# Performance work log

Measured on AMD Instinct MI355X. Metric: run time of the kernel, lower is better.

Reference implementation:

```python
import jax, jax.numpy as jnp
import numpy as np

B, P, N = 64, 100, 1000
D, H, QD = 128, 8, 16
NUM_PATCHES = 196
NTOT = N + NUM_PATCHES
SQRT_D = float(np.sqrt(D))   # sqrt_embedding_dim
CLIP = 10.0                  # logit_clipping


def setup_inputs() -> dict:
    key = jax.random.key(0)
    ks = jax.random.split(key, 10)
    return {
        "encoded_last_node": jax.random.normal(ks[0], (B, P, D), jnp.float32),
        "ninf_mask": jnp.zeros((B, P, N), jnp.float32),
        "q_first": jax.random.normal(ks[1], (B, H, P, QD), jnp.float32),
        "k": jax.random.normal(ks[2], (B, H, NTOT, QD), jnp.float32),
        "v": jax.random.normal(ks[3], (B, H, NTOT, QD), jnp.float32),
        "single_head_key": jax.random.normal(ks[4], (B, D, N), jnp.float32),
        "Wq_last": jax.random.normal(ks[5], (D, H * QD), jnp.float32) * 0.05,
        "mh_combine": jax.random.normal(ks[6], (H * QD, D), jnp.float32) * 0.05,
        "edge_bias": jax.random.normal(ks[7], (B, N, N), jnp.float32) * 0.1,
        "current_node": jax.random.randint(ks[8], (B, P), 0, N, jnp.int64),
        "num_patches": NUM_PATCHES,
    }


def reference(encoded_last_node, ninf_mask, q_first, k, v, single_head_key,
              Wq_last, mh_combine, edge_bias, current_node, num_patches):
    b, p, _ = encoded_last_node.shape
    h, qd = q_first.shape[1], q_first.shape[3]

    # q_last = reshape_by_heads(F.linear(x, Wq_last_para))  -> [B,H,P,qd]
    q_last = (encoded_last_node @ Wq_last.T).reshape(b, p, h, qd).transpose(0, 2, 1, 3)
    q = q_first + q_last

    # multi-head attention with mask extended by zero columns for patch tokens
    mask_full = jnp.pad(ninf_mask, ((0, 0), (0, 0), (0, num_patches)))  # [B,P,Ntot]
    score = jnp.einsum('bhpd,bhnd->bhpn', q, k) / jnp.sqrt(jnp.float32(qd))
    weights = jax.nn.softmax(score + mask_full[:, None, :, :], axis=-1)
    out = jnp.einsum('bhpn,bhnd->bhpd', weights, v)
    out_concat = out.transpose(0, 2, 1, 3).reshape(b, p, h * qd)  # [B,P,D]

    mh_atten_out = out_concat @ mh_combine.T                       # [B,P,D]

    # pointer-style single-head score with tanh clipping
    score2 = jnp.einsum('bpd,bdn->bpn', mh_atten_out, single_head_key)
    score_clipped = CLIP * jnp.tanh(score2 / SQRT_D)

    # gather edge bias row for current node: bias[b,p,n] = edge_bias[b, current_node[b,p], n]
    bias_row = jnp.take_along_axis(edge_bias, current_node[:, :, None], axis=1)
    probs = jax.nn.softmax(score_clipped + bias_row + ninf_mask, axis=-1)
    return probs
```

## Files before the change

### kernel.cpp

```cpp
#include <hip/hip_runtime.h>
#include <math.h>

#define BB 64
#define PP 100
#define NN 1000
#define DD 128
#define HH 8
#define QDQ 16
#define NTOT 1196
#define QROWS 16
#define LOG2E 1.44269504088896f
#define EXP2(x) __builtin_amdgcn_exp2f(x)

typedef float f2 __attribute__((ext_vector_type(2)));
typedef short s8v __attribute__((ext_vector_type(8)));
typedef float f16v __attribute__((ext_vector_type(16)));

static __device__ __forceinline__ f2 splat2(float v) { f2 r; r.x = v; r.y = v; return r; }
#define PKFMA(a, b, c) __builtin_elementwise_fma((a), (b), (c))

static __device__ __forceinline__ unsigned pkhi(float a, float b) {
  return (__float_as_uint(a) >> 16) | (__float_as_uint(b) & 0xffff0000u);
}
static __device__ __forceinline__ float truncbf(float a) {
  return __uint_as_float(__float_as_uint(a) & 0xffff0000u);
}
#define MFMA32(a, b, c) __builtin_amdgcn_mfma_f32_32x32x16_bf16((a), (b), (c), 0, 0, 0)

__global__ __launch_bounds__(256) void k_prep(const float* __restrict__ x,
                                              const float* __restrict__ Wq,
                                              const float* __restrict__ qf,
                                              float* __restrict__ qout,
                                              const float* __restrict__ mask,
                                              unsigned short* __restrict__ m2) {
  __shared__ float sw[128 * 65];
  __shared__ float xs[QROWS * DD];
  int tid = threadIdx.x;

  if (blockIdx.x < 400) {
    int row0 = blockIdx.x * QROWS;
    for (int i = tid; i < QROWS * DD / 4; i += 256)
      ((float4*)xs)[i] = ((const float4*)(x + (size_t)row0 * DD))[i];

    int j = tid & 127, rr = tid >> 7;
    float acc[8];
#pragma unroll
    for (int i = 0; i < 8; ++i) acc[i] = 0.f;

    for (int half = 0; half < 2; ++half) {
      __syncthreads();
      for (int idx = tid; idx < 128 * 64; idx += 256) {
        int jj = idx >> 6, dl = idx & 63;
        sw[jj * 65 + dl] = Wq[jj * DD + half * 64 + dl];
      }
      __syncthreads();
#pragma unroll
      for (int ri = 0; ri < 8; ++ri) {
        int r = 2 * ri + rr;
        float a = acc[ri];
#pragma unroll 16
        for (int dl = 0; dl < 64; ++dl)
          a += xs[r * DD + half * 64 + dl] * sw[j * 65 + dl];
        acc[ri] = a;
      }
    }
#pragma unroll
    for (int ri = 0; ri < 8; ++ri) {
      int bp = row0 + 2 * ri + rr;
      int b = bp / PP, p = bp % PP;
      int h = j >> 4, qd = j & 15;
      size_t qi = ((size_t)(b * HH + h) * PP + p) * QDQ + qd;
      qout[qi] = acc[ri] + qf[qi];
    }
  } else {
    int t2 = blockIdx.x - 400;
    int b = t2 >> 7, q = t2 & 127;
    unsigned short* dst = m2 + (size_t)(b * 128 + q) * 1280;
    const float* srow = mask + ((size_t)b * PP + (q < PP ? q : PP - 1)) * NN;
    for (int j = tid; j < 1280; j += 256) {
      int h = j >= 640 ? 1 : 0;
      int jj = j - h * 640;
      float val;
      if (q >= PP || jj >= 598) {
        val = -1e4f;
      } else {
        int n = h * 598 + jj;
        val = (n < NN) ? srow[n] * LOG2E - 20.f : -20.f;
      }
      dst[j] = (unsigned short)(__float_as_uint(val) >> 16);
    }
  }
}

__global__ __launch_bounds__(256) void k_mha(const float* __restrict__ kk,
                                             const float* __restrict__ vv,
                                             const float* __restrict__ qws,
                                             const unsigned short* __restrict__ m2,
                                             float* __restrict__ part) {
  int bid = blockIdx.x;
  int swz = (bid & 7) * 128 + (bid >> 3);
  int bh = swz >> 1, half = swz & 1;
  int b = bh >> 3;
  int tid = threadIdx.x;
  int w = tid >> 6, lane = tid & 63;
  int L = lane >> 5, ln = lane & 31;
  bool lo = (L == 0);

  __shared__ __align__(16) char pool[27264];
  char* KspB = pool;
  char* VThB = pool + 8192;
  char* VTlB = pool + 12288;
  char* QhB  = pool + 16384;
  char* QlB  = pool + 20480;

  {
    const float* qrow = qws + (size_t)bh * (PP * QDQ);
    for (int i = tid; i < 128 * 16; i += 256) {
      int p = i >> 4, qd = i & 15;
      float v = (p < PP) ? qrow[p * QDQ + qd] * (0.25f * LOG2E) : 0.f;
      ((unsigned short*)QhB)[i] = (unsigned short)(__float_as_uint(v) >> 16);
      float rl = v - truncbf(v);
      ((unsigned short*)QlB)[i] = (unsigned short)(__float_as_uint(rl) >> 16);
    }
  }

  const float4* kf4 = (const float4*)kk + (size_t)bh * NTOT * 4;
  const float4* vf4 = (const float4*)vv + (size_t)bh * NTOT * 4;

  f16v Oacc[4];
  float lacc[4];
#pragma unroll
  for (int qt = 0; qt < 4; ++qt) {
    lacc[qt] = 0.f;
#pragma unroll
    for (int r = 0; r < 16; ++r) Oacc[qt][r] = 0.f;
  }
  s8v QhF[4], QlF[4];

  for (int c = 0; c < 5; ++c) {
    __syncthreads();
#pragma unroll
    for (int rep = 0; rep < 2; ++rep) {
      int f = tid + rep * 256;
      int key_l = f >> 2, qd0 = (f & 3) << 2;
      int j = c * 128 + key_l;
      int jc = j < 598 ? j : 597;
      size_t gidx = (size_t)(half * 598 + jc) * 4 + (qd0 >> 2);
      float4 k4 = kf4[gidx];
      unsigned kh01 = pkhi(k4.x, k4.y), kh23 = pkhi(k4.z, k4.w);
      float r0 = k4.x - truncbf(k4.x), r1 = k4.y - truncbf(k4.y);
      float r2 = k4.z - truncbf(k4.z), r3 = k4.w - truncbf(k4.w);
      unsigned kl01 = pkhi(r0, r1), kl23 = pkhi(r2, r3);
      *(uint2*)(KspB + key_l * 64 + qd0 * 2) = make_uint2(kh01, kh23);
      *(uint2*)(KspB + key_l * 64 + 32 + qd0 * 2) = make_uint2(kl01, kl23);
      float4 v4 = vf4[gidx];
      float ve0 = v4.x, ve1 = v4.y, ve2 = v4.z, ve3 = v4.w;
      ((unsigned short*)VThB)[(qd0 + 0) * 128 + key_l] = (unsigned short)(__float_as_uint(ve0) >> 16);
      ((unsigned short*)VThB)[(qd0 + 1) * 128 + key_l] = (unsigned short)(__float_as_uint(ve1) >> 16);
      ((unsigned short*)VThB)[(qd0 + 2) * 128 + key_l] = (unsigned short)(__float_as_uint(ve2) >> 16);
      ((unsigned short*)VThB)[(qd0 + 3) * 128 + key_l] = (unsigned short)(__float_as_uint(ve3) >> 16);
      float w0 = ve0 - truncbf(ve0), w1 = ve1 - truncbf(ve1);
      float w2 = ve2 - truncbf(ve2), w3 = ve3 - truncbf(ve3);
      ((unsigned short*)VTlB)[(qd0 + 0) * 128 + key_l] = (unsigned short)(__float_as_uint(w0) >> 16);
      ((unsigned short*)VTlB)[(qd0 + 1) * 128 + key_l] = (unsigned short)(__float_as_uint(w1) >> 16);
      ((unsigned short*)VTlB)[(qd0 + 2) * 128 + key_l] = (unsigned short)(__float_as_uint(w2) >> 16);
      ((unsigned short*)VTlB)[(qd0 + 3) * 128 + key_l] = (unsigned short)(__float_as_uint(w3) >> 16);
    }
    __syncthreads();
    if (c == 0) {
#pragma unroll
      for (int qt = 0; qt < 4; ++qt) {
        int qr = qt * 32 + ln;
        QhF[qt] = *(const s8v*)(QhB + qr * 32 + L * 16);
        QlF[qt] = *(const s8v*)(QlB + qr * 32 + L * 16);
      }
    }
    int ktb = w * 32;
    s8v KhF = *(const s8v*)(KspB + (ktb + ln) * 64 + L * 16);
    s8v KlF = *(const s8v*)(KspB + (ktb + ln) * 64 + 32 + L * 16);
    int vr = ln & 15;
    s8v VhS0 = *(const s8v*)(VThB + vr * 256 + (ktb + L * 8) * 2);
    s8v VhS1 = *(const s8v*)(VThB + vr * 256 + (ktb + 16 + L * 8) * 2);
    s8v VlS0 = *(const s8v*)(VTlB + vr * 256 + (ktb + L * 8) * 2);
    s8v VlS1 = *(const s8v*)(VTlB + vr * 256 + (ktb + 16 + L * 8) * 2);
    size_t mkey = (size_t)half * 640 + c * 128 + ktb + 4 * L;
#pragma unroll
    for (int qt = 0; qt < 4; ++qt) {
      const unsigned short* mrow = m2 + (size_t)(b * 128 + qt * 32 + ln) * 1280 + mkey;
      f16v acc;
#pragma unroll
      for (int g = 0; g < 4; ++g) {
        uint2 md = *(const uint2*)(mrow + g * 8);
        acc[g * 4 + 0] = __uint_as_float(md.x << 16);
        acc[g * 4 + 1] = __uint_as_float(md.x & 0xffff0000u);
        acc[g * 4 + 2] = __uint_as_float(md.y << 16);
        acc[g * 4 + 3] = __uint_as_float(md.y & 0xffff0000u);
      }
      acc = MFMA32(KhF, QhF[qt], acc);
      acc = MFMA32(KhF, QlF[qt], acc);
      acc = MFMA32(KlF, QhF[qt], acc);
      float p[16];
      float ls = 0.f;
#pragma unroll
      for (int r = 0; r < 16; ++r) { p[r] = EXP2(acc[r]); ls += p[r]; }
      lacc[qt] += ls;
#pragma unroll
      for (int s = 0; s < 2; ++s) {
        unsigned a0 = pkhi(p[8 * s + 0], p[8 * s + 1]), a1 = pkhi(p[8 * s + 2], p[8 * s + 3]);
        unsigned b0 = pkhi(p[8 * s + 4], p[8 * s + 5]), b1 = pkhi(p[8 * s + 6], p[8 * s + 7]);
        unsigned sa0 = __shfl_xor(a0, 32), sa1 = __shfl_xor(a1, 32);
        unsigned sb0 = __shfl_xor(b0, 32), sb1 = __shfl_xor(b1, 32);
        uint4 phu = make_uint4(lo ? a0 : sb0, lo ? a1 : sb1, lo ? sa0 : b0, lo ? sa1 : b1);
        float t0 = p[8 * s + 0] - truncbf(p[8 * s + 0]), t1 = p[8 * s + 1] - truncbf(p[8 * s + 1]);
        float t2 = p[8 * s + 2] - truncbf(p[8 * s + 2]), t3 = p[8 * s + 3] - truncbf(p[8 * s + 3]);
        float t4 = p[8 * s + 4] - truncbf(p[8 * s + 4]), t5 = p[8 * s + 5] - truncbf(p[8 * s + 5]);
        float t6 = p[8 * s + 6] - truncbf(p[8 * s + 6]), t7 = p[8 * s + 7] - truncbf(p[8 * s + 7]);
        unsigned c0 = pkhi(t0, t1), c1 = pkhi(t2, t3);
        unsigned e0 = pkhi(t4, t5), e1 = pkhi(t6, t7);
        unsigned sc0 = __shfl_xor(c0, 32), sc1 = __shfl_xor(c1, 32);
        unsigned se0 = __shfl_xor(e0, 32), se1 = __shfl_xor(e1, 32);
        uint4 plu = make_uint4(lo ? c0 : se0, lo ? c1 : se1, lo ? sc0 : e0, lo ? sc1 : e1);
        s8v APh = *(s8v*)&phu;
        s8v APl = *(s8v*)&plu;
        s8v Vh = s ? VhS1 : VhS0;
        s8v Vl = s ? VlS1 : VlS0;
        Oacc[qt] = MFMA32(APh, Vh, Oacc[qt]);
        Oacc[qt] = MFMA32(APh, Vl, Oacc[qt]);
        Oacc[qt] = MFMA32(APl, Vh, Oacc[qt]);
      }
    }
  }

  float lf[4];
#pragma unroll
  for (int qt = 0; qt < 4; ++qt) lf[qt] = lacc[qt] + __shfl_xor(lacc[qt], 32);

  __syncthreads();
  float* marea = (float*)pool;
  float* larea = (float*)(pool + 25600);
  if (ln < 16) {
#pragma unroll
    for (int qt = 0; qt < 4; ++qt) {
#pragma unroll
      for (int r = 0; r < 16; ++r) {
        int q = qt * 32 + (r & 3) + 8 * (r >> 2) + 4 * L;
        if (q < PP) marea[(w * PP + q) * 16 + ln] = Oacc[qt][r];
      }
    }
  }
  if (lane < 32) {
#pragma unroll
    for (int qt = 0; qt < 4; ++qt) {
      int q = qt * 32 + ln;
      if (q < PP) larea[w * PP + q] = lf[qt];
    }
  }
  __syncthreads();
  for (int idx = tid; idx < PP * 17; idx += 256) {
    int q = idx / 17, e = idx % 17;
    float sv;
    if (e < 16)
      sv = marea[(0 * PP + q) * 16 + e] + marea[(1 * PP + q) * 16 + e]
         + marea[(2 * PP + q) * 16 + e] + marea[(3 * PP + q) * 16 + e];
    else
      sv = larea[0 * PP + q] + larea[1 * PP + q] + larea[2 * PP + q] + larea[3 * PP + q];
    part[((size_t)swz * PP + q) * 17 + e] = sv;
  }
}

__global__ __launch_bounds__(256) void k_combine(const float* __restrict__ part,
                                                 const float* __restrict__ MC,
                                                 float* __restrict__ mh) {
  __shared__ float sw[128 * 65];
  __shared__ float oc[QROWS * DD];
  int tid = threadIdx.x;
  int row0 = blockIdx.x * QROWS;

  for (int i = tid; i < QROWS * DD; i += 256) {
    int r = i >> 7, t = i & 127;
    int bp = row0 + r, b = bp / PP, p = bp % PP;
    int qd = t & 15, h = t >> 4;
    int bh = b * HH + h;
    const float* r0 = part + (((size_t)(bh * 2 + 0)) * PP + p) * 17;
    const float* r1 = part + (((size_t)(bh * 2 + 1)) * PP + p) * 17;
    float A = r0[qd] + r1[qd];
    float L = r0[16] + r1[16];
    oc[i] = A / L;
  }

  int j = tid & 127, rr = tid >> 7;
  float acc[8];
#pragma unroll
  for (int i = 0; i < 8; ++i) acc[i] = 0.f;

  for (int half = 0; half < 2; ++half) {
    __syncthreads();
    for (int idx = tid; idx < 128 * 64; idx += 256) {
      int jj = idx >> 6, dl = idx & 63;
      sw[jj * 65 + dl] = MC[jj * DD + half * 64 + dl];
    }
    __syncthreads();
#pragma unroll
    for (int ri = 0; ri < 8; ++ri) {
      int r = 2 * ri + rr;
      float a = acc[ri];
#pragma unroll 16
      for (int dl = 0; dl < 64; ++dl)
        a += oc[r * DD + half * 64 + dl] * sw[j * 65 + dl];
      acc[ri] = a;
    }
  }
#pragma unroll
  for (int ri = 0; ri < 8; ++ri) {
    int bp = row0 + 2 * ri + rr;
    mh[(size_t)bp * DD + j] = acc[ri];
  }
}

__global__ __launch_bounds__(256) void k_score2(const float* __restrict__ mh,
                                                const float* __restrict__ shk,
                                                float* __restrict__ sc) {
  int bid = blockIdx.x;
  int swz = (bid & 7) * 128 + (bid >> 3);
  int b = swz >> 4, nt = swz & 15;
  int tid = threadIdx.x; int nl = tid & 31, pg = tid >> 5;
  __shared__ float A[PP * 132];
  for (int idx = tid; idx < PP * DD; idx += 256)
    A[(idx >> 7) * 132 + (idx & 127)] = mh[(size_t)b * PP * DD + idx];
  __syncthreads();

  int na = nt * 64 + nl, nb2 = na + 32;
  int nca = na < NN ? na : NN - 1, ncb = nb2 < NN ? nb2 : NN - 1;
  const float* S = shk + (size_t)b * DD * NN;
  f2 accv[13];
#pragma unroll
  for (int i = 0; i < 13; ++i) accv[i] = splat2(0.f);

  for (int d = 0; d < DD; d += 4) {
    f2 s0, s1, s2, s3;
    s0.x = S[(size_t)(d + 0) * NN + nca]; s0.y = S[(size_t)(d + 0) * NN + ncb];
    s1.x = S[(size_t)(d + 1) * NN + nca]; s1.y = S[(size_t)(d + 1) * NN + ncb];
    s2.x = S[(size_t)(d + 2) * NN + nca]; s2.y = S[(size_t)(d + 2) * NN + ncb];
    s3.x = S[(size_t)(d + 3) * NN + nca]; s3.y = S[(size_t)(d + 3) * NN + ncb];
#pragma unroll
    for (int i = 0; i < 13; ++i) {
      int p = pg + (i << 3);
      if (p < PP) {
        const float4 a4 = *(const float4*)&A[p * 132 + d];
        accv[i] = PKFMA(splat2(a4.x), s0, accv[i]);
        accv[i] = PKFMA(splat2(a4.y), s1, accv[i]);
        accv[i] = PKFMA(splat2(a4.z), s2, accv[i]);
        accv[i] = PKFMA(splat2(a4.w), s3, accv[i]);
      }
    }
  }
#pragma unroll
  for (int i = 0; i < 13; ++i) {
    int p = pg + (i << 3);
    if (p < PP) {
      size_t base = ((size_t)b * PP + p) * NN;
      if (na < NN) sc[base + na] = accv[i].x;
      if (nb2 < NN) sc[base + nb2] = accv[i].y;
    }
  }
}

__global__ __launch_bounds__(256) void k_finsm(const float* __restrict__ sc,
                                               const float* __restrict__ eb,
                                               const int* __restrict__ cn,
                                               const float* __restrict__ mask,
                                               float* __restrict__ out) {
  int bid = blockIdx.x;
  int bp = (bid & 7) * 800 + (bid >> 3);
  int b = bp / PP;
  int t = threadIdx.x;
  int node = cn[bp];
  const float* scp = sc + (size_t)bp * NN;
  const float* ebp = eb + ((size_t)b * NN + node) * NN;
  const float* mp = mask + (size_t)bp * NN;
  const float inv_sqrtD = 0.08838834764831845f;

  float vals[4];
  float s = 0.f;
#pragma unroll
  for (int i = 0; i < 4; ++i) {
    int n = t + (i << 8);
    if (n < NN) {
      float z = scp[n] * inv_sqrtD;
      float e = EXP2(2.f * LOG2E * z);
      float th10 = 10.f - 20.f * __builtin_amdgcn_rcpf(e + 1.f);
      float lg = th10 + ebp[n] + mp[n];
      float e2 = EXP2(lg * LOG2E);
      vals[i] = e2;
      s += e2;
    } else {
      vals[i] = 0.f;
    }
  }
#pragma unroll
  for (int off = 32; off; off >>= 1) s += __shfl_xor(s, off);
  __shared__ float red[4];
  int w = t >> 6, lane = t & 63;
  if (lane == 0) red[w] = s;
  __syncthreads();
  s = (red[0] + red[1]) + (red[2] + red[3]);
  float inv = 1.f / s;
#pragma unroll
  for (int i = 0; i < 4; ++i) {
    int n = t + (i << 8);
    if (n < NN) out[(size_t)bp * NN + n] = vals[i] * inv;
  }
}

extern "C" void kernel_launch(void* const* d_in, const int* in_sizes, int n_in,
                              void* d_out, int out_size, void* d_ws, size_t ws_size,
                              hipStream_t stream) {
  const float* x    = (const float*)d_in[0];
  const float* mask = (const float*)d_in[1];
  const float* qf   = (const float*)d_in[2];
  const float* kk   = (const float*)d_in[3];
  const float* vv   = (const float*)d_in[4];
  const float* shk  = (const float*)d_in[5];
  const float* Wq   = (const float*)d_in[6];
  const float* MC   = (const float*)d_in[7];
  const float* eb   = (const float*)d_in[8];
  const int*   cn   = (const int*)d_in[9];

  float* out = (float*)d_out;
  float* ws = (float*)d_ws;
  float* q_ws = ws;
  float* part = ws + 819200;
  float* mh   = ws + 2560000;
  float* reg  = ws + 3379200;
  unsigned short* m2 = (unsigned short*)reg;
  float* sc   = reg;

  hipLaunchKernelGGL(k_prep, dim3(8592), dim3(256), 0, stream, x, Wq, qf, q_ws, mask, m2);
  hipLaunchKernelGGL(k_mha, dim3(1024), dim3(256), 0, stream, kk, vv, q_ws, m2, part);
  hipLaunchKernelGGL(k_combine, dim3(400), dim3(256), 0, stream, part, MC, mh);
  hipLaunchKernelGGL(k_score2, dim3(1024), dim3(256), 0, stream, mh, shk, sc);
  hipLaunchKernelGGL(k_finsm, dim3(6400), dim3(256), 0, stream, sc, eb, cn, mask, out);
}
```

Measured before the change: 200.0 us.

## Pre-swizzle mask into MFMA fragment order and prefetch next K/V chunk

```diff
diff --git a/kernel.cpp b/kernel.cpp
--- a/kernel.cpp
+++ b/kernel.cpp
@@ -32,7 +32,7 @@
                                               const float* __restrict__ qf,
                                               float* __restrict__ qout,
                                               const float* __restrict__ mask,
-                                              unsigned short* __restrict__ m2) {
+                                              unsigned short* __restrict__ m3) {
   __shared__ float sw[128 * 65];
   __shared__ float xs[QROWS * DD];
   int tid = threadIdx.x;
@@ -74,20 +74,23 @@
     }
   } else {
     int t2 = blockIdx.x - 400;
-    int b = t2 >> 7, q = t2 & 127;
-    unsigned short* dst = m2 + (size_t)(b * 128 + q) * 1280;
-    const float* srow = mask + ((size_t)b * PP + (q < PP ? q : PP - 1)) * NN;
-    for (int j = tid; j < 1280; j += 256) {
-      int h = j >= 640 ? 1 : 0;
-      int jj = j - h * 640;
+    int b = t2 / 10, rem = t2 % 10;
+    int half = rem / 5, c = rem % 5;
+    unsigned short* dst = m3 + (size_t)t2 * 16384;
+    const float* mb = mask + (size_t)b * PP * NN;
+    for (int idx = tid; idx < 16384; idx += 256) {
+      int e = idx & 3, L = (idx >> 2) & 1, lnn = (idx >> 3) & 31;
+      int g = (idx >> 8) & 3, qt = (idx >> 10) & 3, w = (idx >> 12) & 3;
+      int q = qt * 32 + lnn;
+      int local = c * 128 + w * 32 + 4 * L + 8 * g + e;
       float val;
-      if (q >= PP || jj >= 598) {
+      if (q >= PP || local >= 598) {
         val = -1e4f;
       } else {
-        int n = h * 598 + jj;
-        val = (n < NN) ? srow[n] * LOG2E - 20.f : -20.f;
-      }
-      dst[j] = (unsigned short)(__float_as_uint(val) >> 16);
+        int n = half * 598 + local;
+        val = (n < NN) ? mb[(size_t)q * NN + n] * LOG2E - 20.f : -20.f;
+      }
+      dst[idx] = (unsigned short)(__float_as_uint(val) >> 16);
     }
   }
 }
@@ -95,7 +98,7 @@
 __global__ __launch_bounds__(256) void k_mha(const float* __restrict__ kk,
                                              const float* __restrict__ vv,
                                              const float* __restrict__ qws,
-                                             const unsigned short* __restrict__ m2,
+                                             const unsigned short* __restrict__ m3,
                                              float* __restrict__ part) {
   int bid = blockIdx.x;
   int swz = (bid & 7) * 128 + (bid >> 3);
@@ -106,27 +109,50 @@
   int L = lane >> 5, ln = lane & 31;
   bool lo = (L == 0);
 
-  __shared__ __align__(16) char pool[27264];
+  __shared__ __align__(16) char pool[30976];
   char* KspB = pool;
-  char* VThB = pool + 8192;
-  char* VTlB = pool + 12288;
-  char* QhB  = pool + 16384;
-  char* QlB  = pool + 20480;
+  char* VTB  = pool + 10240;
+  char* QhB  = pool + 18688;
+  char* QlB  = pool + 24832;
 
   {
     const float* qrow = qws + (size_t)bh * (PP * QDQ);
-    for (int i = tid; i < 128 * 16; i += 256) {
-      int p = i >> 4, qd = i & 15;
-      float v = (p < PP) ? qrow[p * QDQ + qd] * (0.25f * LOG2E) : 0.f;
-      ((unsigned short*)QhB)[i] = (unsigned short)(__float_as_uint(v) >> 16);
-      float rl = v - truncbf(v);
-      ((unsigned short*)QlB)[i] = (unsigned short)(__float_as_uint(rl) >> 16);
+    const float sc0 = 0.25f * LOG2E;
+    for (int i = tid; i < 512; i += 256) {
+      int p = i >> 2, qd0 = (i & 3) * 4;
+      float4 q4 = make_float4(0.f, 0.f, 0.f, 0.f);
+      if (p < PP) q4 = *(const float4*)(qrow + p * QDQ + qd0);
+      q4.x *= sc0; q4.y *= sc0; q4.z *= sc0; q4.w *= sc0;
+      *(uint2*)(QhB + p * 48 + qd0 * 2) = make_uint2(pkhi(q4.x, q4.y), pkhi(q4.z, q4.w));
+      float r0 = q4.x - truncbf(q4.x), r1 = q4.y - truncbf(q4.y);
+      float r2 = q4.z - truncbf(q4.z), r3 = q4.w - truncbf(q4.w);
+      *(uint2*)(QlB + p * 48 + qd0 * 2) = make_uint2(pkhi(r0, r1), pkhi(r2, r3));
     }
   }
 
   const float4* kf4 = (const float4*)kk + (size_t)bh * NTOT * 4;
   const float4* vf4 = (const float4*)vv + (size_t)bh * NTOT * 4;
 
+#define GLOAD(c, rep, k4v, v4v) { \
+    int f = tid + (rep) * 256; \
+    int jl = (c) * 128 + (f >> 2); jl = jl < 598 ? jl : 597; \
+    size_t gidx = (size_t)(half * 598 + jl) * 4 + (f & 3); \
+    k4v = kf4[gidx]; v4v = vf4[gidx]; }
+
+#define STORE1(rep, k4v, v4v) { \
+    int f = tid + (rep) * 256; \
+    int key_l = f >> 2, qd0 = (f & 3) * 4; \
+    unsigned h0 = pkhi(k4v.x, k4v.y), h1 = pkhi(k4v.z, k4v.w); \
+    float r0 = k4v.x - truncbf(k4v.x), r1 = k4v.y - truncbf(k4v.y); \
+    float r2 = k4v.z - truncbf(k4v.z), r3 = k4v.w - truncbf(k4v.w); \
+    *(uint2*)(KspB + key_l * 80 + qd0 * 2) = make_uint2(h0, h1); \
+    *(uint2*)(KspB + key_l * 80 + 32 + qd0 * 2) = make_uint2(pkhi(r0, r1), pkhi(r2, r3)); \
+    float* vt = (float*)VTB; \
+    vt[(qd0 + 0) * 132 + key_l] = v4v.x; \
+    vt[(qd0 + 1) * 132 + key_l] = v4v.y; \
+    vt[(qd0 + 2) * 132 + key_l] = v4v.z; \
+    vt[(qd0 + 3) * 132 + key_l] = v4v.w; }
+
   f16v Oacc[4];
   float lacc[4];
 #pragma unroll
@@ -137,60 +163,65 @@
   }
   s8v QhF[4], QlF[4];
 
+  float4 k4a, v4a, k4b, v4b;
+  GLOAD(0, 0, k4a, v4a)
+  GLOAD(0, 1, k4b, v4b)
+
   for (int c = 0; c < 5; ++c) {
     __syncthreads();
-#pragma unroll
-    for (int rep = 0; rep < 2; ++rep) {
-      int f = tid + rep * 256;
-      int key_l = f >> 2, qd0 = (f & 3) << 2;
-      int j = c * 128 + key_l;
-      int jc = j < 598 ? j : 597;
-      size_t gidx = (size_t)(half * 598 + jc) * 4 + (qd0 >> 2);
-      float4 k4 = kf4[gidx];
-      unsigned kh01 = pkhi(k4.x, k4.y), kh23 = pkhi(k4.z, k4.w);
-      float r0 = k4.x - truncbf(k4.x), r1 = k4.y - truncbf(k4.y);
-      float r2 = k4.z - truncbf(k4.z), r3 = k4.w - truncbf(k4.w);
-      unsigned kl01 = pkhi(r0, r1), kl23 = pkhi(r2, r3);
-      *(uint2*)(KspB + key_l * 64 + qd0 * 2) = make_uint2(kh01, kh23);
-      *(uint2*)(KspB + key_l * 64 + 32 + qd0 * 2) = make_uint2(kl01, kl23);
-      float4 v4 = vf4[gidx];
-      float ve0 = v4.x, ve1 = v4.y, ve2 = v4.z, ve3 = v4.w;
-      ((unsigned short*)VThB)[(qd0 + 0) * 128 + key_l] = (unsigned short)(__float_as_uint(ve0) >> 16);
-      ((unsigned short*)VThB)[(qd0 + 1) * 128 + key_l] = (unsigned short)(__float_as_uint(ve1) >> 16);
-      ((unsigned short*)VThB)[(qd0 + 2) * 128 + key_l] = (unsigned short)(__float_as_uint(ve2) >> 16);
-      ((unsigned short*)VThB)[(qd0 + 3) * 128 + key_l] = (unsigned short)(__float_as_uint(ve3) >> 16);
-      float w0 = ve0 - truncbf(ve0), w1 = ve1 - truncbf(ve1);
-      float w2 = ve2 - truncbf(ve2), w3 = ve3 - truncbf(ve3);
-      ((unsigned short*)VTlB)[(qd0 + 0) * 128 + key_l] = (unsigned short)(__float_as_uint(w0) >> 16);
-      ((unsigned short*)VTlB)[(qd0 + 1) * 128 + key_l] = (unsigned short)(__float_as_uint(w1) >> 16);
-      ((unsigned short*)VTlB)[(qd0 + 2) * 128 + key_l] = (unsigned short)(__float_as_uint(w2) >> 16);
-      ((unsigned short*)VTlB)[(qd0 + 3) * 128 + key_l] = (unsigned short)(__float_as_uint(w3) >> 16);
-    }
+    STORE1(0, k4a, v4a)
+    STORE1(1, k4b, v4b)
     __syncthreads();
+    if (c < 4) {
+      GLOAD(c + 1, 0, k4a, v4a)
+      GLOAD(c + 1, 1, k4b, v4b)
+    }
     if (c == 0) {
 #pragma unroll
       for (int qt = 0; qt < 4; ++qt) {
         int qr = qt * 32 + ln;
-        QhF[qt] = *(const s8v*)(QhB + qr * 32 + L * 16);
-        QlF[qt] = *(const s8v*)(QlB + qr * 32 + L * 16);
-      }
-    }
+        QhF[qt] = *(const s8v*)(QhB + qr * 48 + L * 16);
+        QlF[qt] = *(const s8v*)(QlB + qr * 48 + L * 16);
+      }
+    }
+
     int ktb = w * 32;
-    s8v KhF = *(const s8v*)(KspB + (ktb + ln) * 64 + L * 16);
-    s8v KlF = *(const s8v*)(KspB + (ktb + ln) * 64 + 32 + L * 16);
+    s8v KhF = *(const s8v*)(KspB + (ktb + ln) * 80 + L * 16);
+    s8v KlF = *(const s8v*)(KspB + (ktb + ln) * 80 + 32 + L * 16);
+
     int vr = ln & 15;
-    s8v VhS0 = *(const s8v*)(VThB + vr * 256 + (ktb + L * 8) * 2);
-    s8v VhS1 = *(const s8v*)(VThB + vr * 256 + (ktb + 16 + L * 8) * 2);
-    s8v VlS0 = *(const s8v*)(VTlB + vr * 256 + (ktb + L * 8) * 2);
-    s8v VlS1 = *(const s8v*)(VTlB + vr * 256 + (ktb + 16 + L * 8) * 2);
-    size_t mkey = (size_t)half * 640 + c * 128 + ktb + 4 * L;
+    const float* vtr = (const float*)VTB + vr * 132;
+    float4 va0 = *(const float4*)(vtr + ktb + L * 8);
+    float4 va1 = *(const float4*)(vtr + ktb + L * 8 + 4);
+    float4 vb0 = *(const float4*)(vtr + ktb + 16 + L * 8);
+    float4 vb1 = *(const float4*)(vtr + ktb + 16 + L * 8 + 4);
+    uint4 vh0u = make_uint4(pkhi(va0.x, va0.y), pkhi(va0.z, va0.w),
+                            pkhi(va1.x, va1.y), pkhi(va1.z, va1.w));
+    uint4 vh1u = make_uint4(pkhi(vb0.x, vb0.y), pkhi(vb0.z, vb0.w),
+                            pkhi(vb1.x, vb1.y), pkhi(vb1.z, vb1.w));
+    float wa0 = va0.x - truncbf(va0.x), wa1 = va0.y - truncbf(va0.y);
+    float wa2 = va0.z - truncbf(va0.z), wa3 = va0.w - truncbf(va0.w);
+    float wa4 = va1.x - truncbf(va1.x), wa5 = va1.y - truncbf(va1.y);
+    float wa6 = va1.z - truncbf(va1.z), wa7 = va1.w - truncbf(va1.w);
+    uint4 vl0u = make_uint4(pkhi(wa0, wa1), pkhi(wa2, wa3), pkhi(wa4, wa5), pkhi(wa6, wa7));
+    float wb0 = vb0.x - truncbf(vb0.x), wb1 = vb0.y - truncbf(vb0.y);
+    float wb2 = vb0.z - truncbf(vb0.z), wb3 = vb0.w - truncbf(vb0.w);
+    float wb4 = vb1.x - truncbf(vb1.x), wb5 = vb1.y - truncbf(vb1.y);
+    float wb6 = vb1.z - truncbf(vb1.z), wb7 = vb1.w - truncbf(vb1.w);
+    uint4 vl1u = make_uint4(pkhi(wb0, wb1), pkhi(wb2, wb3), pkhi(wb4, wb5), pkhi(wb6, wb7));
+    s8v VhS0 = *(s8v*)&vh0u, VhS1 = *(s8v*)&vh1u;
+    s8v VlS0 = *(s8v*)&vl0u, VlS1 = *(s8v*)&vl1u;
+
+    int lanep = (ln << 1) | L;
+    const unsigned short* m3c =
+        m3 + (size_t)((((b * 2 + half) * 5 + c) * 4 + w)) * 4096 + lanep * 4;
 #pragma unroll
     for (int qt = 0; qt < 4; ++qt) {
-      const unsigned short* mrow = m2 + (size_t)(b * 128 + qt * 32 + ln) * 1280 + mkey;
+      const unsigned short* mq = m3c + qt * 1024;
       f16v acc;
 #pragma unroll
       for (int g = 0; g < 4; ++g) {
-        uint2 md = *(const uint2*)(mrow + g * 8);
+        uint2 md = *(const uint2*)(mq + g * 256);
         acc[g * 4 + 0] = __uint_as_float(md.x << 16);
         acc[g * 4 + 1] = __uint_as_float(md.x & 0xffff0000u);
         acc[g * 4 + 2] = __uint_as_float(md.y << 16);
@@ -266,6 +297,8 @@
       sv = larea[0 * PP + q] + larea[1 * PP + q] + larea[2 * PP + q] + larea[3 * PP + q];
     part[((size_t)swz * PP + q) * 17 + e] = sv;
   }
+#undef GLOAD
+#undef STORE1
 }
 
 __global__ __launch_bounds__(256) void k_combine(const float* __restrict__ part,
@@ -432,11 +465,11 @@
   float* part = ws + 819200;
   float* mh   = ws + 2560000;
   float* reg  = ws + 3379200;
-  unsigned short* m2 = (unsigned short*)reg;
+  unsigned short* m3 = (unsigned short*)reg;
   float* sc   = reg;
 
-  hipLaunchKernelGGL(k_prep, dim3(8592), dim3(256), 0, stream, x, Wq, qf, q_ws, mask, m2);
-  hipLaunchKernelGGL(k_mha, dim3(1024), dim3(256), 0, stream, kk, vv, q_ws, m2, part);
+  hipLaunchKernelGGL(k_prep, dim3(1040), dim3(256), 0, stream, x, Wq, qf, q_ws, mask, m3);
+  hipLaunchKernelGGL(k_mha, dim3(1024), dim3(256), 0, stream, kk, vv, q_ws, m3, part);
   hipLaunchKernelGGL(k_combine, dim3(400), dim3(256), 0, stream, part, MC, mh);
   hipLaunchKernelGGL(k_score2, dim3(1024), dim3(256), 0, stream, mh, shk, sc);
   hipLaunchKernelGGL(k_finsm, dim3(6400), dim3(256), 0, stream, sc, eb, cn, mask, out);
```

After: 212.8 us. 1.06x slower.
